# Performance work log

Hardware: AMD Instinct MI355X
Metric: run time of the kernel (lower is better)

## Reference

```python
import jax, jax.numpy as jnp
import numpy as np

V = 49152      # HEALPix nside=64 pixel count
B = 2
FIN = 32
FOUT = 64
K = 8          # Chebyshev kernel_size
DEG = 8        # neighbors per pixel (plus self-loop -> 9 nnz/row)
G = 8          # GroupNorm num_groups
EPS = 1e-5
SLOPE = 0.1    # LeakyReLU negative slope


def setup_inputs() -> dict:
    key = jax.random.key(0)
    ks = jax.random.split(key, 4)
    rng = np.random.default_rng(0)
    # sparse Laplacian in COO: 8 random neighbors + self-loop per node
    row = np.repeat(np.arange(V, dtype=np.int32), DEG + 1)
    nbrs = rng.integers(0, V, size=(V, DEG))
    col = np.concatenate([nbrs, np.arange(V)[:, None]], axis=1).astype(np.int32).reshape(-1)
    vals = (rng.standard_normal(V * (DEG + 1)).astype(np.float32)) * 0.1
    x = jax.random.normal(ks[0], (B, V, FIN), dtype=jnp.float32)
    W1 = jax.random.normal(ks[1], (K, FIN, FOUT), dtype=jnp.float32) * 0.05
    W2 = jax.random.normal(ks[2], (K, FOUT, FOUT), dtype=jnp.float32) * 0.05
    Wr = jax.random.normal(ks[3], (K, FIN, FOUT), dtype=jnp.float32) * 0.05
    zeros = jnp.zeros((FOUT,), dtype=jnp.float32)
    ones = jnp.ones((FOUT,), dtype=jnp.float32)
    return {
        "x": x,
        "lap_vals": jnp.asarray(vals),
        "lap_row": jnp.asarray(row),
        "lap_col": jnp.asarray(col),
        "W1": W1, "b1": zeros, "g1": ones, "be1": zeros,
        "W2": W2, "b2": zeros, "g2": ones, "be2": zeros,
        "Wr": Wr, "br": zeros,
    }


def _spmm(vals, row, col, z):
    # L @ z for COO Laplacian; z: [V, D]
    return jax.ops.segment_sum(vals[:, None] * z[col], row, num_segments=V)


def _cheb_conv(x, vals, row, col, W, b):
    # x: [B, V, Fin], W: [K, Fin, Fout] -> [B, V, Fout]
    Bb, Vv, F = x.shape
    x0 = jnp.transpose(x, (1, 0, 2)).reshape(Vv, Bb * F)  # [V, B*F]
    xs = [x0, _spmm(vals, row, col, x0)]
    for _ in range(K - 2):
        xs.append(2.0 * _spmm(vals, row, col, xs[-1]) - xs[-2])
    Xk = jnp.stack(xs, 0).reshape(K, Vv, Bb, F)
    Xk = jnp.transpose(Xk, (2, 1, 0, 3))  # [B, V, K, F]
    return jnp.einsum('bvkf,kfo->bvo', Xk, W) + b


def _group_norm(x, gamma, beta):
    # equivalent to nn.GroupNorm applied on x.permute(0,2,1): normalize over (C/G, V)
    Bb, Vv, C = x.shape
    xg = x.reshape(Bb, Vv, G, C // G)
    mu = xg.mean(axis=(1, 3), keepdims=True)
    var = xg.var(axis=(1, 3), keepdims=True)
    xn = ((xg - mu) * jax.lax.rsqrt(var + EPS)).reshape(Bb, Vv, C)
    return xn * gamma + beta


def _block(x, vals, row, col, W, b, gamma, beta):
    h = _cheb_conv(x, vals, row, col, W, b)
    h = _group_norm(h, gamma, beta)
    return jax.nn.leaky_relu(h, SLOPE)  # out_channels > 1 -> LeakyReLU(0.1)


def reference(x, lap_vals, lap_row, lap_col, W1, b1, g1, be1, W2, b2, g2, be2, Wr, br):
    h = _block(x, lap_vals, lap_row, lap_col, W1, b1, g1, be1)
    h = _block(h, lap_vals, lap_row, lap_col, W2, b2, g2, be2)
    res = _cheb_conv(x, lap_vals, lap_row, lap_col, Wr, br)  # in != out -> res_conv
    return h + res
```

## Files before the change

kernel.cpp:

```cpp
#include <hip/hip_runtime.h>
#include <hip/hip_bf16.h>

#define V 49152
#define NNZ 9
#define EPSV 1e-5f
#define SLOPE 0.1f

typedef __attribute__((ext_vector_type(8))) short bf16x8;
typedef __attribute__((ext_vector_type(4))) float f32x4;

__device__ __forceinline__ float lo2f(unsigned u) { return __uint_as_float(u << 16); }
__device__ __forceinline__ float hi2f(unsigned u) { return __uint_as_float(u & 0xffff0000u); }
__device__ __forceinline__ unsigned short f2us(float f) {
    __hip_bfloat16 h = __float2bfloat16(f);
    return *(unsigned short*)&h;
}
__device__ __forceinline__ float us2f(unsigned short u) { return __uint_as_float(((unsigned)u) << 16); }
__device__ __forceinline__ unsigned pk2(float a, float b) {
    return ((unsigned)f2us(a)) | (((unsigned)f2us(b)) << 16);
}

__device__ __forceinline__ void gload_lds16(const void* g, void* l) {
    __builtin_amdgcn_global_load_lds((__attribute__((address_space(1))) void*)g,
                                     (__attribute__((address_space(3))) void*)l, 16, 0, 0);
}

__global__ __launch_bounds__(256) void prep_k(
    const float* __restrict__ W1, const float* __restrict__ Wr, const float* __restrict__ W2,
    unsigned short* __restrict__ Wt1, unsigned short* __restrict__ Wtr, unsigned short* __restrict__ Wt2,
    float* __restrict__ part)
{
    int i = blockIdx.x * 256 + threadIdx.x;
    if (i < 32768) {
        int kk = i >> 12, rem = i & 4095, o = rem >> 6, f = rem & 63;
        Wt2[i] = f2us(W2[kk * 4096 + f * 64 + o]);
    } else if (i < 49152) {
        int j = i - 32768;
        int kk = j >> 11, rem = j & 2047, o = rem >> 5, f = rem & 31;
        Wt1[j] = f2us(W1[kk * 2048 + f * 64 + o]);
    } else if (i < 65536) {
        int j = i - 49152;
        int kk = j >> 11, rem = j & 2047, o = rem >> 5, f = rem & 31;
        Wtr[j] = f2us(Wr[kk * 2048 + f * 64 + o]);
    } else if (i < 66560) {
        part[i - 65536] = 0.f;
    }
}

__global__ __launch_bounds__(256) void reorder_k(const float* __restrict__ x, unsigned* __restrict__ t0) {
    int idx = blockIdx.x * 256 + threadIdx.x;
    int v = idx >> 5, j2 = idx & 31;
    int b = j2 >> 4, f0 = (j2 & 15) * 2;
    const float* p = x + ((size_t)b * V + v) * 32 + f0;
    t0[idx] = pk2(p[0], p[1]);
}

template<int THR, bool FIRST>
__global__ __launch_bounds__(256) void spmm_step(
    const uint4* __restrict__ zc, const uint4* __restrict__ zp, uint4* __restrict__ zn,
    const float* __restrict__ vals, const int* __restrict__ col)
{
    constexpr int L4 = THR * 2;
    int tid = blockIdx.x * 256 + threadIdx.x;
    int v = tid / THR;
    int c = (tid - v * THR) * 2;
    int base = v * NNZ;
    float t[16];
    #pragma unroll
    for (int i = 0; i < 16; ++i) t[i] = 0.f;
    #pragma unroll
    for (int n = 0; n < NNZ; ++n) {
        float a = vals[base + n];
        int cc = col[base + n];
        const uint4* p = zc + (size_t)cc * L4 + c;
        uint4 u0 = p[0];
        uint4 u1 = p[1];
        t[0] += a * lo2f(u0.x); t[1] += a * hi2f(u0.x);
        t[2] += a * lo2f(u0.y); t[3] += a * hi2f(u0.y);
        t[4] += a * lo2f(u0.z); t[5] += a * hi2f(u0.z);
        t[6] += a * lo2f(u0.w); t[7] += a * hi2f(u0.w);
        t[8]  += a * lo2f(u1.x); t[9]  += a * hi2f(u1.x);
        t[10] += a * lo2f(u1.y); t[11] += a * hi2f(u1.y);
        t[12] += a * lo2f(u1.z); t[13] += a * hi2f(u1.z);
        t[14] += a * lo2f(u1.w); t[15] += a * hi2f(u1.w);
    }
    if (!FIRST) {
        const uint4* pp = zp + (size_t)v * L4 + c;
        uint4 p0 = pp[0];
        uint4 p1 = pp[1];
        t[0] = 2.f*t[0] - lo2f(p0.x); t[1] = 2.f*t[1] - hi2f(p0.x);
        t[2] = 2.f*t[2] - lo2f(p0.y); t[3] = 2.f*t[3] - hi2f(p0.y);
        t[4] = 2.f*t[4] - lo2f(p0.z); t[5] = 2.f*t[5] - hi2f(p0.z);
        t[6] = 2.f*t[6] - lo2f(p0.w); t[7] = 2.f*t[7] - hi2f(p0.w);
        t[8]  = 2.f*t[8]  - lo2f(p1.x); t[9]  = 2.f*t[9]  - hi2f(p1.x);
        t[10] = 2.f*t[10] - lo2f(p1.y); t[11] = 2.f*t[11] - hi2f(p1.y);
        t[12] = 2.f*t[12] - lo2f(p1.z); t[13] = 2.f*t[13] - hi2f(p1.z);
        t[14] = 2.f*t[14] - lo2f(p1.w); t[15] = 2.f*t[15] - hi2f(p1.w);
    }
    uint4 r0, r1;
    r0.x = pk2(t[0], t[1]);  r0.y = pk2(t[2], t[3]);
    r0.z = pk2(t[4], t[5]);  r0.w = pk2(t[6], t[7]);
    r1.x = pk2(t[8], t[9]);  r1.y = pk2(t[10], t[11]);
    r1.z = pk2(t[12], t[13]); r1.w = pk2(t[14], t[15]);
    uint4* q = zn + (size_t)v * L4 + c;
    q[0] = r0;
    q[1] = r1;
}

template<int F, int NKK, bool DUAL, bool INIT, bool FINAL>
__global__ __launch_bounds__(256) void mfma_gemm(
    const unsigned short* __restrict__ T,
    const unsigned short* __restrict__ WtA, const unsigned short* __restrict__ WtB,
    const float* __restrict__ biasA, const float* __restrict__ biasB,
    unsigned short* __restrict__ ACC, float* __restrict__ resOut,
    float* __restrict__ part)
{
    constexpr int CPR = F / 4;
    constexpr int FH = F / 32;
    constexpr int RST = 68;
    constexpr int STAGE_SH = NKK * 64 * 2 * F;
    constexpr int TRANS_SH = (DUAL ? 2 : 1) * 2 * 64 * RST * 2;
    constexpr int SH = STAGE_SH > TRANS_SH ? STAGE_SH : TRANS_SH;
    __shared__ unsigned short shraw[SH];
    __shared__ float sGrp[32];

    unsigned short* tile = shraw;
    float* accbuf  = (float*)shraw;
    float* dualbuf = accbuf + 2 * 64 * RST;

    int wv = threadIdx.x >> 6, lane = threadIdx.x & 63;
    int quad = lane >> 4, l15 = lane & 15;
    int v0 = blockIdx.x * 64;
    int ot = wv;

    #pragma unroll
    for (int i = 0; i < 16; ++i) {
        int s = (i * 4 + wv) * 64 + lane;
        int kk = s / (64 * CPR);
        int ws = s - kk * 64 * CPR;
        int row = ws / CPR;
        int cl = ws - row * CPR;
        int cg = (cl & ~7) | ((cl & 7) ^ (row & 7));
        const unsigned short* gp = T + ((size_t)kk * V + v0 + row) * (2 * F) + cg * 8;
        gload_lds16(gp, tile + (size_t)(i * 4 + wv) * 64 * 8);
    }

    bf16x8 bw[NKK][FH];
    bf16x8 bd[NKK][FH];
    #pragma unroll
    for (int kk = 0; kk < NKK; ++kk) {
        #pragma unroll
        for (int fh = 0; fh < FH; ++fh) {
            size_t brow = ((size_t)kk * 64 + ot * 16 + l15) * F + fh * 32 + quad * 8;
            bw[kk][fh] = *(const bf16x8*)(const void*)(WtA + brow);
            if constexpr (DUAL) bd[kk][fh] = *(const bf16x8*)(const void*)(WtB + brow);
        }
    }

    f32x4 acc[4][2];
    f32x4 accd[4][2];
    #pragma unroll
    for (int m = 0; m < 4; ++m)
        #pragma unroll
        for (int b = 0; b < 2; ++b) {
            acc[m][b] = (f32x4){0.f, 0.f, 0.f, 0.f};
            if constexpr (DUAL) accd[m][b] = (f32x4){0.f, 0.f, 0.f, 0.f};
        }

    __syncthreads();

    #pragma unroll
    for (int kk = 0; kk < NKK; ++kk) {
        #pragma unroll
        for (int fh = 0; fh < FH; ++fh) {
            #pragma unroll
            for (int m = 0; m < 4; ++m) {
                int r = m * 16 + l15;
                int rx = r & 7;
                const unsigned short* rbase = tile + ((size_t)kk * 64 + r) * 2 * F;
                #pragma unroll
                for (int b = 0; b < 2; ++b) {
                    int c0 = b * (CPR / 2) + fh * 4 + quad;
                    int s0 = (c0 & ~7) | ((c0 & 7) ^ rx);
                    bf16x8 a = *(const bf16x8*)(const void*)(rbase + s0 * 8);
                    acc[m][b] = __builtin_amdgcn_mfma_f32_16x16x32_bf16(a, bw[kk][fh], acc[m][b], 0, 0, 0);
                    if constexpr (DUAL)
                        accd[m][b] = __builtin_amdgcn_mfma_f32_16x16x32_bf16(a, bd[kk][fh], accd[m][b], 0, 0, 0);
                }
            }
        }
    }

    __syncthreads();

    int o = ot * 16 + l15;
    float bia = FINAL ? biasA[o] : 0.f;
    float biaB = DUAL ? biasB[o] : 0.f;
    #pragma unroll
    for (int m = 0; m < 4; ++m) {
        #pragma unroll
        for (int b = 0; b < 2; ++b) {
            #pragma unroll
            for (int rr = 0; rr < 4; ++rr) {
                int r = m * 16 + quad * 4 + rr;
                accbuf[(b * 64 + r) * RST + o] = acc[m][b][rr] + bia;
                if constexpr (DUAL) dualbuf[(b * 64 + r) * RST + o] = accd[m][b][rr] + biaB;
            }
        }
    }
    if constexpr (FINAL) {
        if (threadIdx.x < 32) sGrp[threadIdx.x] = 0.f;
    }
    __syncthreads();

    #pragma unroll
    for (int j = 0; j < 4; ++j) {
        int cid = threadIdx.x + 256 * j;
        int g = cid & 7, r = (cid >> 3) & 63, b = cid >> 9;
        int o0 = g * 8;
        const float* src = accbuf + (b * 64 + r) * RST + o0;
        float e[8];
        #pragma unroll
        for (int i = 0; i < 8; ++i) e[i] = src[i];
        size_t gidx = ((size_t)b * V + v0 + r) * 64 + o0;
        if constexpr (!INIT) {
            uint4 old = *(const uint4*)(const void*)(ACC + gidx);
            e[0] += lo2f(old.x); e[1] += hi2f(old.x);
            e[2] += lo2f(old.y); e[3] += hi2f(old.y);
            e[4] += lo2f(old.z); e[5] += hi2f(old.z);
            e[6] += lo2f(old.w); e[7] += hi2f(old.w);
        }
        uint4 pk;
        pk.x = pk2(e[0], e[1]); pk.y = pk2(e[2], e[3]);
        pk.z = pk2(e[4], e[5]); pk.w = pk2(e[6], e[7]);
        *(uint4*)(void*)(ACC + gidx) = pk;
        if constexpr (FINAL) {
            float s = 0.f, q = 0.f;
            #pragma unroll
            for (int i = 0; i < 8; ++i) { s += e[i]; q += e[i] * e[i]; }
            atomicAdd(&sGrp[b * 8 + g], s);
            atomicAdd(&sGrp[16 + b * 8 + g], q);
        }
    }
    if constexpr (DUAL) {
        #pragma unroll
        for (int j = 0; j < 8; ++j) {
            int cid = threadIdx.x + 256 * j;
            int oc = cid & 15, r = (cid >> 4) & 63, b = cid >> 10;
            float4 vv = *(const float4*)(const void*)(dualbuf + (b * 64 + r) * RST + oc * 4);
            *(float4*)(void*)(resOut + ((size_t)b * V + v0 + r) * 64 + oc * 4) = vv;
        }
    }
    if constexpr (FINAL) {
        __syncthreads();
        if (threadIdx.x < 16) {
            atomicAdd(&part[threadIdx.x * 2],     sGrp[threadIdx.x]);
            atomicAdd(&part[threadIdx.x * 2 + 1], sGrp[16 + threadIdx.x]);
        }
    }
}

__global__ __launch_bounds__(64) void gn_finalize(const float* __restrict__ part, float* __restrict__ stats) {
    int t = threadIdx.x;
    if (t < 16) {
        const float N = (float)V * 8.f;
        float mean = part[t * 2] / N;
        float var = part[t * 2 + 1] / N - mean * mean;
        stats[t * 2] = mean;
        stats[t * 2 + 1] = rsqrtf(var + EPSV);
    }
}

__global__ __launch_bounds__(256) void gn_apply(const unsigned short* __restrict__ ACC,
                                                const float* __restrict__ stats,
                                                const float* __restrict__ gamma, const float* __restrict__ beta,
                                                unsigned* __restrict__ zout) {
    int idx = blockIdx.x * 256 + threadIdx.x;
    int v = idx >> 6, j2 = idx & 63;
    int b = j2 >> 5, o0 = (j2 & 31) * 2;
    float y[2];
    #pragma unroll
    for (int i = 0; i < 2; ++i) {
        int o = o0 + i;
        int bg = b * 8 + (o >> 3);
        float mean = stats[bg * 2], rstd = stats[bg * 2 + 1];
        float val = us2f(ACC[((size_t)b * V + v) * 64 + o]);
        float t = (val - mean) * rstd * gamma[o] + beta[o];
        y[i] = t > 0.f ? t : SLOPE * t;
    }
    zout[idx] = pk2(y[0], y[1]);
}

__global__ __launch_bounds__(256) void final_out(const unsigned short* __restrict__ ACC,
                                                 float* outres,
                                                 const float* __restrict__ stats,
                                                 const float* __restrict__ gamma, const float* __restrict__ beta) {
    int idx = blockIdx.x * 256 + threadIdx.x;
    int o = idx & 63;
    int b = idx >= V * 64 ? 1 : 0;
    int bg = b * 8 + (o >> 3);
    float mean = stats[bg * 2], rstd = stats[bg * 2 + 1];
    float y = (us2f(ACC[idx]) - mean) * rstd * gamma[o] + beta[o];
    y = y > 0.f ? y : SLOPE * y;
    outres[idx] = y + outres[idx];
}

extern "C" void kernel_launch(void* const* d_in, const int* in_sizes, int n_in,
                              void* d_out, int out_size, void* d_ws, size_t ws_size,
                              hipStream_t stream) {
    const float* x    = (const float*)d_in[0];
    const float* vals = (const float*)d_in[1];
    const int*   col  = (const int*)d_in[3];
    const float* W1   = (const float*)d_in[4];
    const float* b1   = (const float*)d_in[5];
    const float* g1   = (const float*)d_in[6];
    const float* be1  = (const float*)d_in[7];
    const float* W2   = (const float*)d_in[8];
    const float* b2   = (const float*)d_in[9];
    const float* g2   = (const float*)d_in[10];
    const float* be2  = (const float*)d_in[11];
    const float* Wr   = (const float*)d_in[12];
    const float* br   = (const float*)d_in[13];
    float* out = (float*)d_out;

    unsigned short* TS  = (unsigned short*)d_ws;
    unsigned short* ACC = TS + (size_t)4 * V * 128;
    unsigned short* Wt1 = ACC + (size_t)2 * V * 64;
    unsigned short* Wtr = Wt1 + 8 * 64 * 32;
    unsigned short* Wt2 = Wtr + 8 * 64 * 32;
    float* PART1 = (float*)(Wt2 + 8 * 64 * 64);
    float* PART2 = PART1 + 32;
    float* ST1   = PART2 + 32;
    float* ST2   = ST1 + 32;

    prep_k<<<260, 256, 0, stream>>>(W1, Wr, W2, Wt1, Wtr, Wt2, PART1);

    uint4* T1s[8];
    for (int k = 0; k < 8; ++k) T1s[k] = (uint4*)(TS + (size_t)k * V * 64);

    reorder_k<<<V * 32 / 256, 256, 0, stream>>>(x, (unsigned*)T1s[0]);
    spmm_step<4, true><<<V * 4 / 256, 256, 0, stream>>>(T1s[0], nullptr, T1s[1], vals, col);
    for (int k = 2; k < 8; ++k)
        spmm_step<4, false><<<V * 4 / 256, 256, 0, stream>>>(T1s[k-1], T1s[k-2], T1s[k], vals, col);

    mfma_gemm<32, 8, true, true, true><<<V / 64, 256, 0, stream>>>(
        TS, Wt1, Wtr, b1, br, ACC, out, PART1);
    gn_finalize<<<1, 64, 0, stream>>>(PART1, ST1);

    uint4* T2s[4];
    for (int k = 0; k < 4; ++k) T2s[k] = (uint4*)(TS + (size_t)k * V * 128);

    gn_apply<<<V * 64 / 256, 256, 0, stream>>>(ACC, ST1, g1, be1, (unsigned*)T2s[0]);
    spmm_step<8, true><<<V * 8 / 256, 256, 0, stream>>>(T2s[0], nullptr, T2s[1], vals, col);
    spmm_step<8, false><<<V * 8 / 256, 256, 0, stream>>>(T2s[1], T2s[0], T2s[2], vals, col);
    spmm_step<8, false><<<V * 8 / 256, 256, 0, stream>>>(T2s[2], T2s[1], T2s[3], vals, col);

    mfma_gemm<64, 4, false, true, false><<<V / 64, 256, 0, stream>>>(
        TS, Wt2, nullptr, b2, nullptr, ACC, nullptr, PART2);

    spmm_step<8, false><<<V * 8 / 256, 256, 0, stream>>>(T2s[3], T2s[2], T2s[0], vals, col);
    spmm_step<8, false><<<V * 8 / 256, 256, 0, stream>>>(T2s[0], T2s[3], T2s[1], vals, col);
    spmm_step<8, false><<<V * 8 / 256, 256, 0, stream>>>(T2s[1], T2s[0], T2s[2], vals, col);
    spmm_step<8, false><<<V * 8 / 256, 256, 0, stream>>>(T2s[2], T2s[1], T2s[3], vals, col);

    mfma_gemm<64, 4, false, false, true><<<V / 64, 256, 0, stream>>>(
        TS, Wt2 + 4 * 64 * 64, nullptr, b2, nullptr, ACC, nullptr, PART2);
    gn_finalize<<<1, 64, 0, stream>>>(PART2, ST2);

    final_out<<<2 * V * 64 / 256, 256, 0, stream>>>(ACC, out, ST2, g2, be2);
}
```

Baseline: 387.1 us.

## Store all eight Chebyshev terms for block 2 and use one phased GEMM

The second block now keeps all eight Chebyshev terms in a larger workspace instead of a rotating four-buffer ring. A single MFMA GEMM walks them in two LDS phases, replacing two GEMMs that each reread and rewrote the accumulator. The separate gn_finalize launches are removed; gn_apply and final_out compute mean and rstd inline from the partial sums and process eight channels per thread with vector loads and stores. The cost is more workspace memory, and each thread recomputes the group statistics.

```diff
diff --git a/kernel.cpp b/kernel.cpp
--- a/kernel.cpp
+++ b/kernel.cpp
@@ -107,7 +107,7 @@
     q[1] = r1;
 }
 
-template<int F, int NKK, bool DUAL, bool INIT, bool FINAL>
+template<int F, int NKK, int NPH, bool DUAL, bool INIT, bool FINAL>
 __global__ __launch_bounds__(256) void mfma_gemm(
     const unsigned short* __restrict__ T,
     const unsigned short* __restrict__ WtA, const unsigned short* __restrict__ WtB,
@@ -115,10 +115,11 @@
     unsigned short* __restrict__ ACC, float* __restrict__ resOut,
     float* __restrict__ part)
 {
+    constexpr int KPP = NKK / NPH;
     constexpr int CPR = F / 4;
     constexpr int FH = F / 32;
     constexpr int RST = 68;
-    constexpr int STAGE_SH = NKK * 64 * 2 * F;
+    constexpr int STAGE_SH = KPP * 64 * 2 * F;
     constexpr int TRANS_SH = (DUAL ? 2 : 1) * 2 * 64 * RST * 2;
     constexpr int SH = STAGE_SH > TRANS_SH ? STAGE_SH : TRANS_SH;
     __shared__ unsigned short shraw[SH];
@@ -133,59 +134,68 @@
     int v0 = blockIdx.x * 64;
     int ot = wv;
 
-    #pragma unroll
-    for (int i = 0; i < 16; ++i) {
-        int s = (i * 4 + wv) * 64 + lane;
-        int kk = s / (64 * CPR);
-        int ws = s - kk * 64 * CPR;
-        int row = ws / CPR;
-        int cl = ws - row * CPR;
-        int cg = (cl & ~7) | ((cl & 7) ^ (row & 7));
-        const unsigned short* gp = T + ((size_t)kk * V + v0 + row) * (2 * F) + cg * 8;
-        gload_lds16(gp, tile + (size_t)(i * 4 + wv) * 64 * 8);
-    }
-
     bf16x8 bw[NKK][FH];
     bf16x8 bd[NKK][FH];
-    #pragma unroll
-    for (int kk = 0; kk < NKK; ++kk) {
-        #pragma unroll
-        for (int fh = 0; fh < FH; ++fh) {
-            size_t brow = ((size_t)kk * 64 + ot * 16 + l15) * F + fh * 32 + quad * 8;
-            bw[kk][fh] = *(const bf16x8*)(const void*)(WtA + brow);
-            if constexpr (DUAL) bd[kk][fh] = *(const bf16x8*)(const void*)(WtB + brow);
-        }
-    }
-
     f32x4 acc[4][2];
     f32x4 accd[4][2];
-    #pragma unroll
-    for (int m = 0; m < 4; ++m)
-        #pragma unroll
-        for (int b = 0; b < 2; ++b) {
-            acc[m][b] = (f32x4){0.f, 0.f, 0.f, 0.f};
-            if constexpr (DUAL) accd[m][b] = (f32x4){0.f, 0.f, 0.f, 0.f};
-        }
-
-    __syncthreads();
-
-    #pragma unroll
-    for (int kk = 0; kk < NKK; ++kk) {
-        #pragma unroll
-        for (int fh = 0; fh < FH; ++fh) {
-            #pragma unroll
-            for (int m = 0; m < 4; ++m) {
-                int r = m * 16 + l15;
-                int rx = r & 7;
-                const unsigned short* rbase = tile + ((size_t)kk * 64 + r) * 2 * F;
+
+    #pragma unroll
+    for (int ph = 0; ph < NPH; ++ph) {
+        if (ph > 0) __syncthreads();
+
+        #pragma unroll
+        for (int i = 0; i < (KPP * 64 * CPR) / 256; ++i) {
+            int s = (i * 4 + wv) * 64 + lane;
+            int kkl = s / (64 * CPR);
+            int ws = s - kkl * 64 * CPR;
+            int row = ws / CPR;
+            int cl = ws - row * CPR;
+            int cg = (cl & ~7) | ((cl & 7) ^ (row & 7));
+            const unsigned short* gp =
+                T + ((size_t)(ph * KPP + kkl) * V + v0 + row) * (2 * F) + cg * 8;
+            gload_lds16(gp, tile + (size_t)(i * 4 + wv) * 64 * 8);
+        }
+
+        if (ph == 0) {
+            #pragma unroll
+            for (int kk = 0; kk < NKK; ++kk) {
+                #pragma unroll
+                for (int fh = 0; fh < FH; ++fh) {
+                    size_t brow = ((size_t)kk * 64 + ot * 16 + l15) * F + fh * 32 + quad * 8;
+                    bw[kk][fh] = *(const bf16x8*)(const void*)(WtA + brow);
+                    if constexpr (DUAL) bd[kk][fh] = *(const bf16x8*)(const void*)(WtB + brow);
+                }
+            }
+            #pragma unroll
+            for (int m = 0; m < 4; ++m)
                 #pragma unroll
                 for (int b = 0; b < 2; ++b) {
-                    int c0 = b * (CPR / 2) + fh * 4 + quad;
-                    int s0 = (c0 & ~7) | ((c0 & 7) ^ rx);
-                    bf16x8 a = *(const bf16x8*)(const void*)(rbase + s0 * 8);
-                    acc[m][b] = __builtin_amdgcn_mfma_f32_16x16x32_bf16(a, bw[kk][fh], acc[m][b], 0, 0, 0);
-                    if constexpr (DUAL)
-                        accd[m][b] = __builtin_amdgcn_mfma_f32_16x16x32_bf16(a, bd[kk][fh], accd[m][b], 0, 0, 0);
+                    acc[m][b] = (f32x4){0.f, 0.f, 0.f, 0.f};
+                    if constexpr (DUAL) accd[m][b] = (f32x4){0.f, 0.f, 0.f, 0.f};
+                }
+        }
+
+        __syncthreads();
+
+        #pragma unroll
+        for (int kkl = 0; kkl < KPP; ++kkl) {
+            int kk = ph * KPP + kkl;
+            #pragma unroll
+            for (int fh = 0; fh < FH; ++fh) {
+                #pragma unroll
+                for (int m = 0; m < 4; ++m) {
+                    int r = m * 16 + l15;
+                    int rx = r & 7;
+                    const unsigned short* rbase = tile + ((size_t)kkl * 64 + r) * 2 * F;
+                    #pragma unroll
+                    for (int b = 0; b < 2; ++b) {
+                        int c0 = b * (CPR / 2) + fh * 4 + quad;
+                        int s0 = (c0 & ~7) | ((c0 & 7) ^ rx);
+                        bf16x8 a = *(const bf16x8*)(const void*)(rbase + s0 * 8);
+                        acc[m][b] = __builtin_amdgcn_mfma_f32_16x16x32_bf16(a, bw[kk][fh], acc[m][b], 0, 0, 0);
+                        if constexpr (DUAL)
+                            accd[m][b] = __builtin_amdgcn_mfma_f32_16x16x32_bf16(a, bd[kk][fh], accd[m][b], 0, 0, 0);
+                    }
                 }
             }
         }
@@ -260,49 +270,61 @@
     }
 }
 
-__global__ __launch_bounds__(64) void gn_finalize(const float* __restrict__ part, float* __restrict__ stats) {
-    int t = threadIdx.x;
-    if (t < 16) {
-        const float N = (float)V * 8.f;
-        float mean = part[t * 2] / N;
-        float var = part[t * 2 + 1] / N - mean * mean;
-        stats[t * 2] = mean;
-        stats[t * 2 + 1] = rsqrtf(var + EPSV);
-    }
-}
-
 __global__ __launch_bounds__(256) void gn_apply(const unsigned short* __restrict__ ACC,
-                                                const float* __restrict__ stats,
+                                                const float* __restrict__ part,
                                                 const float* __restrict__ gamma, const float* __restrict__ beta,
                                                 unsigned* __restrict__ zout) {
     int idx = blockIdx.x * 256 + threadIdx.x;
-    int v = idx >> 6, j2 = idx & 63;
-    int b = j2 >> 5, o0 = (j2 & 31) * 2;
-    float y[2];
-    #pragma unroll
-    for (int i = 0; i < 2; ++i) {
-        int o = o0 + i;
-        int bg = b * 8 + (o >> 3);
-        float mean = stats[bg * 2], rstd = stats[bg * 2 + 1];
-        float val = us2f(ACC[((size_t)b * V + v) * 64 + o]);
-        float t = (val - mean) * rstd * gamma[o] + beta[o];
+    int v = idx >> 4, j = idx & 15;
+    int b = j >> 3, g = j & 7;
+    const float N = (float)V * 8.f;
+    float mean = part[j * 2] / N;
+    float rstd = rsqrtf(part[j * 2 + 1] / N - mean * mean + EPSV);
+    int o0 = g * 8;
+    uint4 aa = *(const uint4*)(const void*)(ACC + ((size_t)b * V + v) * 64 + o0);
+    float e[8] = { lo2f(aa.x), hi2f(aa.x), lo2f(aa.y), hi2f(aa.y),
+                   lo2f(aa.z), hi2f(aa.z), lo2f(aa.w), hi2f(aa.w) };
+    float y[8];
+    #pragma unroll
+    for (int i = 0; i < 8; ++i) {
+        float t = (e[i] - mean) * rstd * gamma[o0 + i] + beta[o0 + i];
         y[i] = t > 0.f ? t : SLOPE * t;
     }
-    zout[idx] = pk2(y[0], y[1]);
+    uint4 pk;
+    pk.x = pk2(y[0], y[1]); pk.y = pk2(y[2], y[3]);
+    pk.z = pk2(y[4], y[5]); pk.w = pk2(y[6], y[7]);
+    *(uint4*)(void*)(zout + (size_t)v * 64 + b * 32 + g * 4) = pk;
 }
 
 __global__ __launch_bounds__(256) void final_out(const unsigned short* __restrict__ ACC,
                                                  float* outres,
-                                                 const float* __restrict__ stats,
+                                                 const float* __restrict__ part,
                                                  const float* __restrict__ gamma, const float* __restrict__ beta) {
     int idx = blockIdx.x * 256 + threadIdx.x;
-    int o = idx & 63;
-    int b = idx >= V * 64 ? 1 : 0;
-    int bg = b * 8 + (o >> 3);
-    float mean = stats[bg * 2], rstd = stats[bg * 2 + 1];
-    float y = (us2f(ACC[idx]) - mean) * rstd * gamma[o] + beta[o];
-    y = y > 0.f ? y : SLOPE * y;
-    outres[idx] = y + outres[idx];
+    int b = idx >= V * 8 ? 1 : 0;
+    int r = idx - b * V * 8;
+    int v = r >> 3, g = r & 7;
+    int j = b * 8 + g;
+    const float N = (float)V * 8.f;
+    float mean = part[j * 2] / N;
+    float rstd = rsqrtf(part[j * 2 + 1] / N - mean * mean + EPSV);
+    int o0 = g * 8;
+    size_t base = ((size_t)b * V + v) * 64 + o0;
+    uint4 aa = *(const uint4*)(const void*)(ACC + base);
+    float e[8] = { lo2f(aa.x), hi2f(aa.x), lo2f(aa.y), hi2f(aa.y),
+                   lo2f(aa.z), hi2f(aa.z), lo2f(aa.w), hi2f(aa.w) };
+    float4 r0 = *(const float4*)(const void*)(outres + base);
+    float4 r1 = *(const float4*)(const void*)(outres + base + 4);
+    float y[8];
+    #pragma unroll
+    for (int i = 0; i < 8; ++i) {
+        float t = (e[i] - mean) * rstd * gamma[o0 + i] + beta[o0 + i];
+        y[i] = t > 0.f ? t : SLOPE * t;
+    }
+    float4 w0 = { y[0] + r0.x, y[1] + r0.y, y[2] + r0.z, y[3] + r0.w };
+    float4 w1 = { y[4] + r1.x, y[5] + r1.y, y[6] + r1.z, y[7] + r1.w };
+    *(float4*)(void*)(outres + base) = w0;
+    *(float4*)(void*)(outres + base + 4) = w1;
 }
 
 extern "C" void kernel_launch(void* const* d_in, const int* in_sizes, int n_in,
@@ -324,14 +346,12 @@
     float* out = (float*)d_out;
 
     unsigned short* TS  = (unsigned short*)d_ws;
-    unsigned short* ACC = TS + (size_t)4 * V * 128;
+    unsigned short* ACC = TS + (size_t)8 * V * 128;
     unsigned short* Wt1 = ACC + (size_t)2 * V * 64;
     unsigned short* Wtr = Wt1 + 8 * 64 * 32;
     unsigned short* Wt2 = Wtr + 8 * 64 * 32;
     float* PART1 = (float*)(Wt2 + 8 * 64 * 64);
     float* PART2 = PART1 + 32;
-    float* ST1   = PART2 + 32;
-    float* ST2   = ST1 + 32;
 
     prep_k<<<260, 256, 0, stream>>>(W1, Wr, W2, Wt1, Wtr, Wt2, PART1);
 
@@ -343,29 +363,19 @@
     for (int k = 2; k < 8; ++k)
         spmm_step<4, false><<<V * 4 / 256, 256, 0, stream>>>(T1s[k-1], T1s[k-2], T1s[k], vals, col);
 
-    mfma_gemm<32, 8, true, true, true><<<V / 64, 256, 0, stream>>>(
+    mfma_gemm<32, 8, 1, true, true, true><<<V / 64, 256, 0, stream>>>(
         TS, Wt1, Wtr, b1, br, ACC, out, PART1);
-    gn_finalize<<<1, 64, 0, stream>>>(PART1, ST1);
-
-    uint4* T2s[4];
-    for (int k = 0; k < 4; ++k) T2s[k] = (uint4*)(TS + (size_t)k * V * 128);
-
-    gn_apply<<<V * 64 / 256, 256, 0, stream>>>(ACC, ST1, g1, be1, (unsigned*)T2s[0]);
+
+    uint4* T2s[8];
+    for (int k = 0; k < 8; ++k) T2s[k] = (uint4*)(TS + (size_t)k * V * 128);
+
+    gn_apply<<<V * 16 / 256, 256, 0, stream>>>(ACC, PART1, g1, be1, (unsigned*)T2s[0]);
     spmm_step<8, true><<<V * 8 / 256, 256, 0, stream>>>(T2s[0], nullptr, T2s[1], vals, col);
-    spmm_step<8, false><<<V * 8 / 256, 256, 0, stream>>>(T2s[1], T2s[0], T2s[2], vals, col);
-    spmm_step<8, false><<<V * 8 / 256, 256, 0, stream>>>(T2s[2], T2s[1], T2s[3], vals, col);
-
-    mfma_gemm<64, 4, false, true, false><<<V / 64, 256, 0, stream>>>(
+    for (int k = 2; k < 8; ++k)
+        spmm_step<8, false><<<V * 8 / 256, 256, 0, stream>>>(T2s[k-1], T2s[k-2], T2s[k], vals, col);
+
+    mfma_gemm<64, 8, 2, false, true, true><<<V / 64, 256, 0, stream>>>(
         TS, Wt2, nullptr, b2, nullptr, ACC, nullptr, PART2);
 
-    spmm_step<8, false><<<V * 8 / 256, 256, 0, stream>>>(T2s[3], T2s[2], T2s[0], vals, col);
-    spmm_step<8, false><<<V * 8 / 256, 256, 0, stream>>>(T2s[0], T2s[3], T2s[1], vals, col);
-    spmm_step<8, false><<<V * 8 / 256, 256, 0, stream>>>(T2s[1], T2s[0], T2s[2], vals, col);
-    spmm_step<8, false><<<V * 8 / 256, 256, 0, stream>>>(T2s[2], T2s[1], T2s[3], vals, col);
-
-    mfma_gemm<64, 4, false, false, true><<<V / 64, 256, 0, stream>>>(
-        TS, Wt2 + 4 * 64 * 64, nullptr, b2, nullptr, ACC, nullptr, PART2);
-    gn_finalize<<<1, 64, 0, stream>>>(PART2, ST2);
-
-    final_out<<<2 * V * 64 / 256, 256, 0, stream>>>(ACC, out, ST2, g2, be2);
-}
+    final_out<<<2 * V * 8 / 256, 256, 0, stream>>>(ACC, out, PART2, g2, be2);
+}
```

Result: faster. 366.5 us (-5.3%).
